# Kernel tuning notes

Measured on AMD Instinct MI355X. Metric: run time of the kernel, lower is better.

Reference implementation:

```python
import jax, jax.numpy as jnp
import numpy as np
from jax import lax

N_GROUPS, TOP_K, CALIB_SCALE = 4, 3, 2.0


def setup_inputs() -> dict:
    key = jax.random.key(0)
    ks = jax.random.split(key, 32)
    d = {}
    d['x'] = jax.random.normal(ks[0], (64, 64, 8192), jnp.float32)
    d['conv_weight'] = jax.random.normal(ks[1], (64, 64, 3), jnp.float32) * 0.05
    d['bias'] = jax.random.normal(ks[2], (64,), jnp.float32) * 0.05
    d['grads'] = jax.random.normal(ks[3], (12288,), jnp.float32) * 0.01
    d['q_ema'] = jax.random.normal(ks[4], (4416,), jnp.float32) * 0.1
    d['ctrl_w'] = jax.random.normal(ks[5], (64, 192), jnp.float32) * 0.07
    d['ctrl_b'] = jnp.zeros((64,), jnp.float32)
    d['gp_w'] = jax.random.normal(ks[6], (64, 65), jnp.float32) * 0.1
    d['gp_b'] = jnp.zeros((64,), jnp.float32)
    d['gt_w'] = jax.random.normal(ks[7], (64, 64), jnp.float32) * 0.1
    d['gt_b'] = jnp.zeros((64,), jnp.float32)
    d['ln_g'] = jnp.ones((64,), jnp.float32)
    d['ln_b'] = jnp.zeros((64,), jnp.float32)
    d['ccin_w'] = jax.random.normal(ks[8], (64, 64), jnp.float32) * 0.05
    d['ccin_b'] = jnp.zeros((64,), jnp.float32)
    d['ck_w'] = jax.random.normal(ks[9], (3, 64), jnp.float32) * 0.05
    d['ck_b'] = jnp.zeros((3,), jnp.float32)
    d['cb_w'] = jax.random.normal(ks[10], (1, 64), jnp.float32) * 0.05
    d['cb_b'] = jnp.zeros((1,), jnp.float32)
    d['cf_w'] = jax.random.normal(ks[11], (1, 64), jnp.float32) * 0.05
    d['cf_b'] = jnp.zeros((1,), jnp.float32)
    d['tau_w'] = jax.random.normal(ks[12], (1, 64), jnp.float32) * 0.1
    d['tau_b'] = jnp.zeros((1,), jnp.float32)
    W = jax.random.normal(ks[13], (4, 1104, 32), jnp.float32)
    d['mem_W'] = W / jnp.linalg.norm(W, axis=1, keepdims=True)  # column-normalized codebook
    d['temp_logit'] = jnp.zeros((4,), jnp.float32)
    return d


def reference(x, conv_weight, bias, grads, q_ema, ctrl_w, ctrl_b, gp_w, gp_b,
              gt_w, gt_b, ln_g, ln_b, ccin_w, ccin_b, ck_w, ck_b, cb_w, cb_b,
              cf_w, cf_b, tau_w, tau_b, mem_W, temp_logit):
    C_out, C_in, K = conv_weight.shape
    cpg = C_out // N_GROUPS
    cin_tot, k_tot = C_out * C_in, C_out * K
    shift = 0.0  # shift_magnitude

    # --- controller: grads -> calibration query q ---
    g = grads.reshape(C_out, C_in * K)
    h = jax.nn.silu(g @ ctrl_w.T + ctrl_b)
    gn = jnp.linalg.norm(g, axis=-1, keepdims=True)
    z = jax.nn.sigmoid(jnp.concatenate([h, gn], -1) @ gp_w.T + gp_b)
    h_t = jax.nn.silu(h @ gt_w.T + gt_b)
    hm = (1.0 - z) * h + z * h_t
    mu = hm.mean(-1, keepdims=True)
    var = ((hm - mu) ** 2).mean(-1, keepdims=True)
    h = ln_g * (hm - mu) / jnp.sqrt(var + 1e-5) + ln_b

    w_cin = jnp.tanh(h @ ccin_w.T + ccin_b) * CALIB_SCALE   # [C_out, C_in]
    w_k = jnp.tanh(h @ ck_w.T + ck_b) * CALIB_SCALE         # [C_out, K]
    b_r = jnp.tanh(h @ cb_w.T + cb_b)[:, 0] * CALIB_SCALE   # [C_out]
    f_r = jnp.tanh(h @ cf_w.T + cf_b)[:, 0] * CALIB_SCALE   # [C_out]
    tau = jax.nn.sigmoid(h @ tau_w.T + tau_b).mean() * 0.5 + 0.5

    q = jnp.concatenate([w_cin.reshape(-1), w_k.reshape(-1), b_r, f_r])
    q = 0.7 * q + 0.3 * lax.stop_gradient(q_ema)

    # --- channel-grouped codebook retrieval (trigger path) ---
    qd = lax.stop_gradient(q)
    q_groups = jnp.concatenate([
        qd[:cin_tot].reshape(N_GROUPS, cpg * C_in),
        qd[cin_tot:cin_tot + k_tot].reshape(N_GROUPS, cpg * K),
        qd[cin_tot + k_tot:cin_tot + k_tot + C_out].reshape(N_GROUPS, cpg),
        qd[cin_tot + k_tot + C_out:].reshape(N_GROUPS, cpg)], axis=1)  # [G, gq]
    temp = (jax.nn.sigmoid(temp_logit) * 0.6 + 0.2) / (1.0 + shift)     # [G]
    att = jnp.einsum('gd,gdm->gm', q_groups, mem_W)
    att = jax.nn.softmax(att / (temp[:, None] + 1e-8), axis=1)
    v, idx = lax.top_k(att, TOP_K)                                      # [G, k]
    gath = jnp.take_along_axis(mem_W, idx[:, None, :], axis=2)          # [G, gq, k]
    retrieved = (gath * v[:, None, :]).sum(-1)                          # [G, gq]

    s0, s1, s2 = cpg * C_in, cpg * (C_in + K), cpg * (C_in + K + 1)
    retrieved_global = jnp.concatenate([
        retrieved[:, :s0].reshape(-1),
        retrieved[:, s0:s1].reshape(-1),
        retrieved[:, s1:s2].reshape(-1),
        retrieved[:, s2:].reshape(-1)])
    q = tau * q + (1.0 - tau) * lax.stop_gradient(retrieved_global)

    # --- split q and modulate conv ---
    w_cin = q[:cin_tot].reshape(C_out, C_in)
    w_k = q[cin_tot:cin_tot + k_tot].reshape(C_out, K)
    b_c = q[cin_tot + k_tot:cin_tot + k_tot + C_out]
    f_c = q[cin_tot + k_tot + C_out:]

    w = conv_weight * (1.0 + w_cin)[:, :, None] * (1.0 + w_k)[:, None, :]
    pad = ((K - 1) * 1 + 1) // 2  # receptive_field // 2 (dilation=1)
    out = lax.conv_general_dilated(x, w, window_strides=(1,),
                                   padding=[(pad, pad)], rhs_dilation=(1,),
                                   dimension_numbers=('NCH', 'OIH', 'NCH'))
    out = out + (bias * (1.0 + b_c))[None, :, None]
    out = out * (1.0 + f_c)[None, :, None]
    return out
```

## Files before the change

### kernel.cpp

```cpp
#include <hip/hip_runtime.h>
#include <math.h>

typedef __attribute__((ext_vector_type(8))) short bf16x8;
typedef __attribute__((ext_vector_type(4))) float f32x4;
typedef unsigned long long ull;

__device__ __forceinline__ float sigmoidf_(float x) { return 1.f / (1.f + expf(-x)); }

__device__ __forceinline__ unsigned f2bf(float f) {
  unsigned int u = __float_as_uint(f);
  u += 0x7fffu + ((u >> 16) & 1u);
  return u >> 16;
}

#define WS_BEFF  0
#define WS_SEFF  64
#define WS_WFRAG 128

__global__ __launch_bounds__(1024) void kCtl(
    const float* __restrict__ grads, const float* __restrict__ ctrl_w, const float* __restrict__ ctrl_b,
    const float* __restrict__ gp_w, const float* __restrict__ gp_b,
    const float* __restrict__ gt_w, const float* __restrict__ gt_b,
    const float* __restrict__ ln_g, const float* __restrict__ ln_b,
    const float* __restrict__ ccin_w, const float* __restrict__ ccin_b,
    const float* __restrict__ ck_w, const float* __restrict__ ck_b,
    const float* __restrict__ cb_w, const float* __restrict__ cb_b,
    const float* __restrict__ cf_w, const float* __restrict__ cf_b,
    const float* __restrict__ tau_w, const float* __restrict__ tau_b,
    const float* __restrict__ q_ema, const float* __restrict__ mem_W,
    const float* __restrict__ temp_logit,
    const float* __restrict__ conv_weight, const float* __restrict__ bias,
    float* __restrict__ ws) {
  __shared__ float rawA[8514];
  __shared__ float sh_h[64 * 65];
  __shared__ float gnp[64 * 17];
  __shared__ float taup[64];
  __shared__ float sh_qg[4416];
  __shared__ float part[16][32];
  __shared__ float sv[3];
  __shared__ int sidx[3];
  __shared__ float qc1[16][64];
  __shared__ float qk1[16][3];
  __shared__ float sh_tau;
  const int tid = threadIdx.x;
  const int g = blockIdx.x;
  const int j = tid & 63;
  const int wv = tid >> 6;
  const int i0 = wv * 4;
  const int i0u = __builtin_amdgcn_readfirstlane(i0);

  float acc[4] = {0.f, 0.f, 0.f, 0.f};
  for (int hh = 0; hh < 2; ++hh) {
    const int d0 = hh * 96;
    for (int t = tid; t < 6144; t += 1024) {
      int jj = t / 96, dl = t - jj * 96;
      rawA[dl * 66 + jj] = ctrl_w[jj * 192 + d0 + dl];
    }
    __syncthreads();
    const float* g0 = grads + i0u * 192 + d0;
#pragma unroll 8
    for (int dl = 0; dl < 96; ++dl) {
      float wvv = rawA[dl * 66 + j];
      acc[0] += wvv * g0[dl];
      acc[1] += wvv * g0[192 + dl];
      acc[2] += wvv * g0[384 + dl];
      acc[3] += wvv * g0[576 + dl];
    }
    __syncthreads();
  }
  {
    float cb_ = ctrl_b[j];
#pragma unroll
    for (int ii = 0; ii < 4; ++ii) {
      float s = acc[ii] + cb_;
      sh_h[(i0 + ii) * 65 + j] = s * sigmoidf_(s);
    }
  }
  {
    int gi = tid >> 4, seg = tid & 15;
    const float* gr = grads + gi * 192 + seg * 12;
    float ss = 0.f;
#pragma unroll
    for (int m = 0; m < 12; ++m) { float v = gr[m]; ss += v * v; }
    gnp[gi * 17 + seg] = ss;
  }
  __syncthreads();
  if (tid < 64) {
    float s = 0.f;
#pragma unroll
    for (int seg = 0; seg < 16; ++seg) s += gnp[tid * 17 + seg];
    gnp[tid * 17 + 16] = sqrtf(s);
  }
  for (int t = tid; t < 4096; t += 1024) rawA[(t & 63) * 66 + (t >> 6)] = gt_w[t];
  for (int t = tid; t < 4160; t += 1024) {
    int jj = t / 65, dd = t - jj * 65;
    rawA[4224 + dd * 66 + jj] = gp_w[t];
  }
  __syncthreads();

  float hm[4];
  {
    float zacc[4] = {0.f, 0.f, 0.f, 0.f}, tacc[4] = {0.f, 0.f, 0.f, 0.f};
#pragma unroll 4
    for (int d = 0; d < 64; ++d) {
      float gtv = rawA[d * 66 + j];
      float gpv = rawA[4224 + d * 66 + j];
#pragma unroll
      for (int ii = 0; ii < 4; ++ii) {
        float hv = sh_h[(i0 + ii) * 65 + d];
        tacc[ii] += hv * gtv;
        zacc[ii] += hv * gpv;
      }
    }
    float gplast = rawA[4224 + 64 * 66 + j];
    float zb = gp_b[j], tb = gt_b[j];
#pragma unroll
    for (int ii = 0; ii < 4; ++ii) {
      float gn_ = gnp[(i0 + ii) * 17 + 16];
      float zs = zacc[ii] + gn_ * gplast + zb;
      float ts = tacc[ii] + tb;
      float z = sigmoidf_(zs);
      float ht = ts * sigmoidf_(ts);
      hm[ii] = (1.f - z) * sh_h[(i0 + ii) * 65 + j] + z * ht;
    }
  }
  __syncthreads();
#pragma unroll
  for (int ii = 0; ii < 4; ++ii) sh_h[(i0 + ii) * 65 + j] = hm[ii];
  __syncthreads();

  {
    float lg = ln_g[j], lb = ln_b[j];
#pragma unroll
    for (int ii = 0; ii < 4; ++ii) {
      float x = sh_h[(i0 + ii) * 65 + j];
      float s = x;
#pragma unroll
      for (int off = 32; off; off >>= 1) s += __shfl_xor(s, off);
      float mu = s * (1.f / 64.f);
      float dv = x - mu;
      float v2 = dv * dv;
#pragma unroll
      for (int off = 32; off; off >>= 1) v2 += __shfl_xor(v2, off);
      float invs = 1.f / sqrtf(v2 * (1.f / 64.f) + 1e-5f);
      sh_h[(i0 + ii) * 65 + j] = lg * dv * invs + lb;
    }
  }
  for (int t = tid; t < 4096; t += 1024) rawA[(t & 63) * 66 + (t >> 6)] = ccin_w[t];
  if (tid < 384) {
    int c = tid >> 6, d = tid & 63;
    float v = (c < 3) ? ck_w[c * 64 + d] : (c == 3) ? cb_w[d] : (c == 4) ? cf_w[d] : tau_w[d];
    rawA[4224 + c * 64 + d] = v;
  }
  __syncthreads();

  {
    float cb_ = ccin_b[j];
    float s4[4] = {0.f, 0.f, 0.f, 0.f};
#pragma unroll 4
    for (int d = 0; d < 64; ++d) {
      float cv = rawA[d * 66 + j];
#pragma unroll
      for (int ii = 0; ii < 4; ++ii) s4[ii] += sh_h[(i0 + ii) * 65 + d] * cv;
    }
#pragma unroll
    for (int ii = 0; ii < 4; ++ii) {
      int i = i0 + ii;
      float val = 2.f * tanhf(s4[ii] + cb_);
      sh_qg[(i >> 4) * 1104 + (i & 15) * 64 + j] = 0.7f * val + 0.3f * q_ema[i * 64 + j];
    }
  }
  if (wv < 6) {
    int i = j;
    float s = 0.f;
    const float* er = rawA + 4224 + wv * 64;
#pragma unroll 4
    for (int d = 0; d < 64; ++d) s += sh_h[i * 65 + d] * er[d];
    if (wv < 3) {
      float val = 2.f * tanhf(s + ck_b[wv]);
      sh_qg[(i >> 4) * 1104 + 1024 + (i & 15) * 3 + wv] = 0.7f * val + 0.3f * q_ema[4096 + i * 3 + wv];
    } else if (wv == 3) {
      float val = 2.f * tanhf(s + cb_b[0]);
      sh_qg[(i >> 4) * 1104 + 1072 + (i & 15)] = 0.7f * val + 0.3f * q_ema[4288 + i];
    } else if (wv == 4) {
      float val = 2.f * tanhf(s + cf_b[0]);
      sh_qg[(i >> 4) * 1104 + 1088 + (i & 15)] = 0.7f * val + 0.3f * q_ema[4352 + i];
    } else {
      taup[i] = sigmoidf_(s + tau_b[0]);
    }
  }
  __syncthreads();
  if (tid < 64) {
    float t_ = taup[tid];
#pragma unroll
    for (int off = 32; off; off >>= 1) t_ += __shfl_xor(t_, off);
    if (tid == 0) sh_tau = (t_ * (1.f / 64.f)) * 0.5f + 0.5f;
  }
  __syncthreads();

  const float* mwg = mem_W + (size_t)g * 1104 * 32;
  {
    float4 a = {0.f, 0.f, 0.f, 0.f};
    const float* qg = sh_qg + g * 1104;
#pragma unroll
    for (int it = 0; it < 9; ++it) {
      int d = it * 128 + (tid >> 3);
      if (d < 1104) {
        float4 v4 = *(const float4*)(mwg + (size_t)d * 32 + (tid & 7) * 4);
        float qv = qg[d];
        a.x += qv * v4.x; a.y += qv * v4.y; a.z += qv * v4.z; a.w += qv * v4.w;
      }
    }
#pragma unroll
    for (int off = 8; off <= 32; off <<= 1) {
      a.x += __shfl_xor(a.x, off); a.y += __shfl_xor(a.y, off);
      a.z += __shfl_xor(a.z, off); a.w += __shfl_xor(a.w, off);
    }
    if ((tid & 63) < 8) *(float4*)&part[tid >> 6][(tid & 7) * 4] = a;
  }
  __syncthreads();

  if (tid < 32) {
    int m = tid;
    float att = 0.f;
#pragma unroll
    for (int w = 0; w < 16; ++w) att += part[w][m];
    float temp = 0.6f * sigmoidf_(temp_logit[g]) + 0.2f;
    att /= (temp + 1e-8f);
    float mx = att;
#pragma unroll
    for (int off = 16; off; off >>= 1) mx = fmaxf(mx, __shfl_xor(mx, off, 32));
    float e = expf(att - mx);
    float s = e;
#pragma unroll
    for (int off = 16; off; off >>= 1) s += __shfl_xor(s, off, 32);
    float p = e / s;
    for (int t = 0; t < 3; ++t) {
      float bp = p; int bm = m;
#pragma unroll
      for (int off = 16; off; off >>= 1) {
        float op = __shfl_xor(bp, off, 32);
        int om = __shfl_xor(bm, off, 32);
        if (op > bp || (op == bp && om < bm)) { bp = op; bm = om; }
      }
      if (m == 0) { sv[t] = bp; sidx[t] = bm; }
      if (m == bm) p = -1.f;
    }
  }
  __syncthreads();

  {
    const float tau = sh_tau;
    const float v0 = sv[0], v1 = sv[1], v2 = sv[2];
    const int x0 = sidx[0], x1 = sidx[1], x2 = sidx[2];
    const float* qg = sh_qg + g * 1104;
    int cl = wv;
    int co = 16 * g + cl;
    int lane = j;
    {
      int d = cl * 64 + lane;
      float r = v0 * mwg[(size_t)d * 32 + x0] + v1 * mwg[(size_t)d * 32 + x1] + v2 * mwg[(size_t)d * 32 + x2];
      qc1[cl][lane] = 1.f + tau * qg[d] + (1.f - tau) * r;
    }
    if (lane < 3) {
      int d = 1024 + cl * 3 + lane;
      float r = v0 * mwg[(size_t)d * 32 + x0] + v1 * mwg[(size_t)d * 32 + x1] + v2 * mwg[(size_t)d * 32 + x2];
      qk1[cl][lane] = 1.f + tau * qg[d] + (1.f - tau) * r;
    }
    if (lane == 3) {
      int d = 1072 + cl;
      float r = v0 * mwg[(size_t)d * 32 + x0] + v1 * mwg[(size_t)d * 32 + x1] + v2 * mwg[(size_t)d * 32 + x2];
      float qb = tau * qg[d] + (1.f - tau) * r;
      ws[WS_BEFF + co] = bias[co] * (1.f + qb);
    }
    if (lane == 4) {
      int d = 1088 + cl;
      float r = v0 * mwg[(size_t)d * 32 + x0] + v1 * mwg[(size_t)d * 32 + x1] + v2 * mwg[(size_t)d * 32 + x2];
      ws[WS_SEFF + co] = 1.f + tau * qg[d] + (1.f - tau) * r;
    }
  }
  __syncthreads();

  unsigned short* wfrag = (unsigned short*)(ws + WS_WFRAG);
  for (int idx = tid; idx < 3072; idx += 1024) {
    int cl = idx / 192, rem = idx - cl * 192;
    int kk = rem >> 6, ci = rem & 63;
    int co = 16 * g + cl;
    float val = conv_weight[(co * 64 + ci) * 3 + kk] * qc1[cl][ci] * qk1[cl][kk];
    int e = kk * 64 + ci;
    int s = e >> 5, hi = (e >> 3) & 3, jj = e & 7;
    wfrag[s * 2048 + g * 512 + (16 * hi + cl) * 8 + jj] = (unsigned short)f2bf(val);
  }
}

__global__ __launch_bounds__(256, 8) void k3_v7nt(
    const float* __restrict__ x, const unsigned short* __restrict__ wfrag,
    const float* __restrict__ beff, const float* __restrict__ seff,
    float* __restrict__ out) {
  __shared__ unsigned short xs[130 * 64];
  const int tid = threadIdx.x;
  const int w = tid >> 6, l = tid & 63;
  const int g = l >> 4, c16 = l & 15;
  const int n = blockIdx.y;
  const int l0 = blockIdx.x * 128;

  bf16x8 wf[6];
#pragma unroll
  for (int s = 0; s < 6; ++s)
    wf[s] = *(const bf16x8*)(wfrag + s * 2048 + w * 512 + l * 8);

  {
    const int cp = 8 * w + (l >> 3);
    const float* r0 = x + ((size_t)(n * 64 + 2 * cp)) * 8192 + l0;
    const float* r1 = r0 + 8192;
    char* xb = (char*)xs;
#pragma unroll
    for (int t = 0; t < 4; ++t) {
      int p0 = 4 * ((l & 7) + 8 * t);
      float4 va = *(const float4*)(r0 + p0);
      float4 vb = *(const float4*)(r1 + p0);
      float av[4] = {va.x, va.y, va.z, va.w};
      float bv[4] = {vb.x, vb.y, vb.z, vb.w};
#pragma unroll
      for (int i = 0; i < 4; ++i) {
        int p = p0 + i + 1;
        unsigned u = f2bf(av[i]) | (f2bf(bv[i]) << 16);
        *(unsigned*)(xb + p * 128 + ((4 * cp) ^ ((p & 7) << 4))) = u;
      }
    }
    if ((l & 7) == 0) {
      float a0 = 0.f, b0 = 0.f, a1 = 0.f, b1 = 0.f;
      if (l0 > 0) {
        float4 va = *(const float4*)(r0 - 4);
        float4 vb = *(const float4*)(r1 - 4);
        a0 = va.w; b0 = vb.w;
      }
      if (l0 + 128 < 8192) {
        float4 va = *(const float4*)(r0 + 128);
        float4 vb = *(const float4*)(r1 + 128);
        a1 = va.x; b1 = vb.x;
      }
      unsigned u0 = f2bf(a0) | (f2bf(b0) << 16);
      unsigned u1 = f2bf(a1) | (f2bf(b1) << 16);
      *(unsigned*)(xb + 0 * 128 + (4 * cp)) = u0;
      *(unsigned*)(xb + 129 * 128 + ((4 * cp) ^ 16)) = u1;
    }
  }
  __syncthreads();

  f32x4 acc[8];
#pragma unroll
  for (int t = 0; t < 8; ++t) acc[t] = (f32x4){0.f, 0.f, 0.f, 0.f};

  const char* xbc = (const char*)xs;
#pragma unroll
  for (int s = 0; s < 6; ++s) {
    const int kk = s >> 1;
    const int C = 4 * (s & 1) + g;
#pragma unroll
    for (int nt = 0; nt < 8; ++nt) {
      const int p = 16 * nt + c16 + kk;
      bf16x8 A = *(const bf16x8*)(xbc + p * 128 + ((C ^ (p & 7)) << 4));
      acc[nt] = __builtin_amdgcn_mfma_f32_16x16x32_bf16(A, wf[s], acc[nt], 0, 0, 0);
    }
  }

  const int co = 16 * w + c16;
  const float be = beff[co], se = seff[co];
  float* orow = out + ((size_t)(n * 64 + co)) * 8192 + l0 + 4 * g;
#pragma unroll
  for (int nt = 0; nt < 8; ++nt) {
    f32x4 ov;
    ov[0] = se * (acc[nt][0] + be);
    ov[1] = se * (acc[nt][1] + be);
    ov[2] = se * (acc[nt][2] + be);
    ov[3] = se * (acc[nt][3] + be);
    __builtin_nontemporal_store(ov, (f32x4*)(orow + nt * 16));
  }
}

extern "C" void kernel_launch(void* const* d_in, const int* in_sizes, int n_in,
                              void* d_out, int out_size, void* d_ws, size_t ws_size,
                              hipStream_t stream) {
  const float* x = (const float*)d_in[0];
  const float* conv_weight = (const float*)d_in[1];
  const float* bias = (const float*)d_in[2];
  const float* grads = (const float*)d_in[3];
  const float* q_ema = (const float*)d_in[4];
  const float* ctrl_w = (const float*)d_in[5];
  const float* ctrl_b = (const float*)d_in[6];
  const float* gp_w = (const float*)d_in[7];
  const float* gp_b = (const float*)d_in[8];
  const float* gt_w = (const float*)d_in[9];
  const float* gt_b = (const float*)d_in[10];
  const float* ln_g = (const float*)d_in[11];
  const float* ln_b = (const float*)d_in[12];
  const float* ccin_w = (const float*)d_in[13];
  const float* ccin_b = (const float*)d_in[14];
  const float* ck_w = (const float*)d_in[15];
  const float* ck_b = (const float*)d_in[16];
  const float* cb_w = (const float*)d_in[17];
  const float* cb_b = (const float*)d_in[18];
  const float* cf_w = (const float*)d_in[19];
  const float* cf_b = (const float*)d_in[20];
  const float* tau_w = (const float*)d_in[21];
  const float* tau_b = (const float*)d_in[22];
  const float* mem_W = (const float*)d_in[23];
  const float* temp_logit = (const float*)d_in[24];

  float* ws = (float*)d_ws;

  hipLaunchKernelGGL(kCtl, dim3(4), dim3(1024), 0, stream,
                     grads, ctrl_w, ctrl_b, gp_w, gp_b, gt_w, gt_b, ln_g, ln_b,
                     ccin_w, ccin_b, ck_w, ck_b, cb_w, cb_b, cf_w, cf_b,
                     tau_w, tau_b, q_ema, mem_W, temp_logit, conv_weight, bias, ws);
  hipLaunchKernelGGL(k3_v7nt, dim3(64, 64), dim3(256), 0, stream,
                     x, (const unsigned short*)(ws + WS_WFRAG), ws + WS_BEFF, ws + WS_SEFF,
                     (float*)d_out);
}
```

Baseline: 108.2 us.

## Stream x tiles into LDS via global_load_lds with double-buffered pipeline

The conv kernel now handles 256 columns per block in four 64-column stages. Raw fp32 x tiles are loaded straight into LDS with async global_load_lds into a double buffer, then converted to bf16 in LDS, so later loads overlap with MFMA work and output stores. Grid size is halved, occupancy drops to 3 blocks per CU with larger LDS use, and nontemporal stores become regular stores. The hand-written waitcnt counts must match the number of outstanding loads exactly, and the extra LDS round trips add cost.

```diff
diff --git a/kernel.cpp b/kernel.cpp
--- a/kernel.cpp
+++ b/kernel.cpp
@@ -293,90 +293,141 @@
   }
 }
 
-__global__ __launch_bounds__(256, 8) void k3_v7nt(
+__global__ __launch_bounds__(256, 3) void k3_dma(
     const float* __restrict__ x, const unsigned short* __restrict__ wfrag,
     const float* __restrict__ beff, const float* __restrict__ seff,
     float* __restrict__ out) {
-  __shared__ unsigned short xs[130 * 64];
+  __shared__ float X[2][64][68];
+  __shared__ unsigned bsu[66 * 32];
+  char* bb = (char*)bsu;
   const int tid = threadIdx.x;
   const int w = tid >> 6, l = tid & 63;
   const int g = l >> 4, c16 = l & 15;
   const int n = blockIdx.y;
-  const int l0 = blockIdx.x * 128;
+  const int base = blockIdx.x * 256;
 
   bf16x8 wf[6];
 #pragma unroll
   for (int s = 0; s < 6; ++s)
     wf[s] = *(const bf16x8*)(wfrag + s * 2048 + w * 512 + l * 8);
-
-  {
-    const int cp = 8 * w + (l >> 3);
-    const float* r0 = x + ((size_t)(n * 64 + 2 * cp)) * 8192 + l0;
-    const float* r1 = r0 + 8192;
-    char* xb = (char*)xs;
-#pragma unroll
-    for (int t = 0; t < 4; ++t) {
-      int p0 = 4 * ((l & 7) + 8 * t);
-      float4 va = *(const float4*)(r0 + p0);
-      float4 vb = *(const float4*)(r1 + p0);
-      float av[4] = {va.x, va.y, va.z, va.w};
-      float bv[4] = {vb.x, vb.y, vb.z, vb.w};
-#pragma unroll
-      for (int i = 0; i < 4; ++i) {
-        int p = p0 + i + 1;
-        unsigned u = f2bf(av[i]) | (f2bf(bv[i]) << 16);
-        *(unsigned*)(xb + p * 128 + ((4 * cp) ^ ((p & 7) << 4))) = u;
-      }
-    }
-    if ((l & 7) == 0) {
-      float a0 = 0.f, b0 = 0.f, a1 = 0.f, b1 = 0.f;
-      if (l0 > 0) {
-        float4 va = *(const float4*)(r0 - 4);
-        float4 vb = *(const float4*)(r1 - 4);
-        a0 = va.w; b0 = vb.w;
-      }
-      if (l0 + 128 < 8192) {
-        float4 va = *(const float4*)(r0 + 128);
-        float4 vb = *(const float4*)(r1 + 128);
-        a1 = va.x; b1 = vb.x;
-      }
-      unsigned u0 = f2bf(a0) | (f2bf(b0) << 16);
-      unsigned u1 = f2bf(a1) | (f2bf(b1) << 16);
-      *(unsigned*)(xb + 0 * 128 + (4 * cp)) = u0;
-      *(unsigned*)(xb + 129 * 128 + ((4 * cp) ^ 16)) = u1;
-    }
-  }
-  __syncthreads();
-
-  f32x4 acc[8];
-#pragma unroll
-  for (int t = 0; t < 8; ++t) acc[t] = (f32x4){0.f, 0.f, 0.f, 0.f};
-
-  const char* xbc = (const char*)xs;
-#pragma unroll
-  for (int s = 0; s < 6; ++s) {
-    const int kk = s >> 1;
-    const int C = 4 * (s & 1) + g;
-#pragma unroll
-    for (int nt = 0; nt < 8; ++nt) {
-      const int p = 16 * nt + c16 + kk;
-      bf16x8 A = *(const bf16x8*)(xbc + p * 128 + ((C ^ (p & 7)) << 4));
-      acc[nt] = __builtin_amdgcn_mfma_f32_16x16x32_bf16(A, wf[s], acc[nt], 0, 0, 0);
-    }
-  }
-
+  __builtin_amdgcn_sched_barrier(0);
   const int co = 16 * w + c16;
   const float be = beff[co], se = seff[co];
-  float* orow = out + ((size_t)(n * 64 + co)) * 8192 + l0 + 4 * g;
-#pragma unroll
-  for (int nt = 0; nt < 8; ++nt) {
-    f32x4 ov;
-    ov[0] = se * (acc[nt][0] + be);
-    ov[1] = se * (acc[nt][1] + be);
-    ov[2] = se * (acc[nt][2] + be);
-    ov[3] = se * (acc[nt][3] + be);
-    __builtin_nontemporal_store(ov, (f32x4*)(orow + nt * 16));
-  }
+  __builtin_amdgcn_sched_barrier(0);
+  const int cb = tid >> 5, cpb = tid & 31;
+  unsigned bndu;
+  {
+    int boff = (cb < 4) ? (64 * cb - 1) : (64 * (cb - 4) + 64);
+    int col = base + boff;
+    int colc = min(max(col, 0), 8191);
+    const float* bp = x + ((size_t)(n * 64 + 2 * cpb)) * 8192 + colc;
+    float f0 = bp[0];
+    float f1 = bp[8192];
+    bndu = (col >= 0 && col < 8192) ? (f2bf(f0) | (f2bf(f1) << 16)) : 0u;
+  }
+  __builtin_amdgcn_sched_barrier(0);
+
+#define GLL(B, POS0)                                                          \
+  {                                                                           \
+    _Pragma("unroll") for (int i_ = 0; i_ < 16; ++i_) {                       \
+      int row_ = 16 * w + i_;                                                 \
+      __builtin_amdgcn_global_load_lds(                                       \
+          (const __attribute__((address_space(1))) void*)(                    \
+              x + ((size_t)(n * 64 + row_)) * 8192 + (POS0) + l),             \
+          (__attribute__((address_space(3))) void*)(&X[B][row_][0]),          \
+          4, 0, 0);                                                           \
+    }                                                                         \
+    __builtin_amdgcn_sched_barrier(0);                                        \
+  }
+
+#define WVM(N)                                                                \
+  __builtin_amdgcn_sched_barrier(0);                                          \
+  asm volatile("s_waitcnt vmcnt(" #N ")" ::: "memory");                       \
+  __builtin_amdgcn_sched_barrier(0);
+
+#define BARX                                                                  \
+  asm volatile("s_waitcnt lgkmcnt(0)" ::: "memory");                          \
+  __builtin_amdgcn_sched_barrier(0);                                          \
+  __builtin_amdgcn_s_barrier();                                               \
+  __builtin_amdgcn_sched_barrier(0);
+
+#define CVT(B, R0, R65)                                                       \
+  {                                                                           \
+    const int cp_ = tid & 31, pg_ = tid >> 5;                                 \
+    float4 a0 = *(const float4*)&X[B][2 * cp_][8 * pg_];                      \
+    float4 a1 = *(const float4*)&X[B][2 * cp_][8 * pg_ + 4];                  \
+    float4 b0 = *(const float4*)&X[B][2 * cp_ + 1][8 * pg_];                  \
+    float4 b1 = *(const float4*)&X[B][2 * cp_ + 1][8 * pg_ + 4];              \
+    float af_[8] = {a0.x, a0.y, a0.z, a0.w, a1.x, a1.y, a1.z, a1.w};          \
+    float bf_[8] = {b0.x, b0.y, b0.z, b0.w, b1.x, b1.y, b1.z, b1.w};          \
+    _Pragma("unroll") for (int i_ = 0; i_ < 8; ++i_) {                        \
+      int p_ = 1 + 8 * pg_ + i_;                                              \
+      unsigned u_ = f2bf(af_[i_]) | (f2bf(bf_[i_]) << 16);                    \
+      *(unsigned*)(bb + p_ * 128 + ((4 * cp_) ^ ((p_ & 7) << 4))) = u_;       \
+    }                                                                         \
+    if (cb == (R0))  *(unsigned*)(bb + 4 * cpb) = bndu;                       \
+    if (cb == (R65)) *(unsigned*)(bb + 65 * 128 + ((4 * cpb) ^ 16)) = bndu;   \
+  }
+
+#define MFMA_ST(T)                                                            \
+  {                                                                           \
+    f32x4 acc_[4];                                                            \
+    _Pragma("unroll") for (int q_ = 0; q_ < 4; ++q_)                          \
+        acc_[q_] = (f32x4){0.f, 0.f, 0.f, 0.f};                               \
+    _Pragma("unroll") for (int s_ = 0; s_ < 6; ++s_) {                        \
+      const int kk_ = s_ >> 1;                                                \
+      const int C_ = 4 * (s_ & 1) + g;                                        \
+      _Pragma("unroll") for (int nt_ = 0; nt_ < 4; ++nt_) {                   \
+        const int p_ = 16 * nt_ + c16 + kk_;                                  \
+        bf16x8 A_ = *(const bf16x8*)(bb + p_ * 128 + ((C_ ^ (p_ & 7)) << 4)); \
+        acc_[nt_] = __builtin_amdgcn_mfma_f32_16x16x32_bf16(A_, wf[s_], acc_[nt_], 0, 0, 0); \
+      }                                                                       \
+    }                                                                         \
+    float* orow_ = out + ((size_t)(n * 64 + co)) * 8192 + base + 64 * (T) + 4 * g; \
+    _Pragma("unroll") for (int nt_ = 0; nt_ < 4; ++nt_) {                     \
+      float4 ov_;                                                             \
+      ov_.x = se * (acc_[nt_][0] + be);                                       \
+      ov_.y = se * (acc_[nt_][1] + be);                                       \
+      ov_.z = se * (acc_[nt_][2] + be);                                       \
+      ov_.w = se * (acc_[nt_][3] + be);                                       \
+      *(float4*)(orow_ + nt_ * 16) = ov_;                                     \
+    }                                                                         \
+  }
+
+  GLL(0, base)
+  GLL(1, base + 64)
+
+  WVM(16)
+  BARX
+  CVT(0, 0, 4)
+  BARX
+  GLL(0, base + 128)
+  MFMA_ST(0)
+
+  WVM(20)
+  BARX
+  CVT(1, 1, 5)
+  BARX
+  GLL(1, base + 192)
+  MFMA_ST(1)
+
+  WVM(24)
+  BARX
+  CVT(0, 2, 6)
+  BARX
+  MFMA_ST(2)
+
+  WVM(8)
+  BARX
+  CVT(1, 3, 7)
+  BARX
+  MFMA_ST(3)
+
+#undef GLL
+#undef WVM
+#undef BARX
+#undef CVT
+#undef MFMA_ST
 }
 
 extern "C" void kernel_launch(void* const* d_in, const int* in_sizes, int n_in,
@@ -414,7 +465,7 @@
                      grads, ctrl_w, ctrl_b, gp_w, gp_b, gt_w, gt_b, ln_g, ln_b,
                      ccin_w, ccin_b, ck_w, ck_b, cb_w, cb_b, cf_w, cf_b,
                      tau_w, tau_b, q_ema, mem_W, temp_logit, conv_weight, bias, ws);
-  hipLaunchKernelGGL(k3_v7nt, dim3(64, 64), dim3(256), 0, stream,
+  hipLaunchKernelGGL(k3_dma, dim3(32, 64), dim3(256), 0, stream,
                      x, (const unsigned short*)(ws + WS_WFRAG), ws + WS_BEFF, ws + WS_SEFF,
                      (float*)d_out);
 }
```

Result: no change. 106.3 us (-1.8%).
